# Kernel tuning notes

Measured on AMD Instinct MI355X. Metric: run time of the kernel, lower is better.

## Reference

```python
import jax, jax.numpy as jnp
import numpy as np

D_MODEL = 1024
NUM_HEADS = 16
MAX_SEQ_LEN = 2048
THETA = 10000.0
HEAD_DIM = D_MODEL // NUM_HEADS  # 64


def _trunc_normal(key, shape, std):
    # truncated normal in [-3, 3] sigma, matching nn.init.trunc_normal_
    return std * jax.random.truncated_normal(key, -3.0, 3.0, shape, dtype=jnp.float32)


def setup_inputs() -> dict:
    key = jax.random.key(0)
    kx, kq, kk, kv, ko = jax.random.split(key, 5)
    B, L = 2, 2048
    sigma = np.sqrt(2.0 / (D_MODEL + D_MODEL))
    x = jax.random.normal(kx, (B, L, D_MODEL), dtype=jnp.float32)
    token_positions = jnp.arange(L, dtype=jnp.int64 if jax.config.jax_enable_x64 else jnp.int32)[None, :]
    return {
        "x": x,
        "wq": _trunc_normal(kq, (D_MODEL, D_MODEL), sigma),
        "wk": _trunc_normal(kk, (D_MODEL, D_MODEL), sigma),
        "wv": _trunc_normal(kv, (D_MODEL, D_MODEL), sigma),
        "wo": _trunc_normal(ko, (D_MODEL, D_MODEL), sigma),
        "token_positions": token_positions,
    }


def _rope_tables():
    pos = jnp.arange(MAX_SEQ_LEN, dtype=jnp.float32)
    d_idx = jnp.arange(HEAD_DIM // 2, dtype=jnp.float32)
    inv_freq = THETA ** (-2.0 * d_idx / HEAD_DIM)
    angles = pos[:, None] * inv_freq[None, :]  # [max_seq_len, head_dim/2]
    return jnp.cos(angles), jnp.sin(angles)


def _apply_rope(x, cos, sin):
    # x: [b, n, l, h]; cos/sin: [1, l, h/2] (broadcast over b, n)
    xe = x[..., 0::2]
    xo = x[..., 1::2]
    oe = cos * xe - sin * xo
    oo = sin * xe + cos * xo
    # interleave back: stack last axis then flatten pairs
    out = jnp.stack([oe, oo], axis=-1)
    return out.reshape(x.shape)


def reference(x, wq, wk, wv, wo, token_positions):
    B, L, _ = x.shape
    cos_t, sin_t = _rope_tables()
    cos = cos_t[token_positions]  # [1, L, h/2]
    sin = sin_t[token_positions]

    def proj(w):
        y = jnp.einsum('bld,ed->ble', x, w)
        return y.reshape(B, L, NUM_HEADS, HEAD_DIM).transpose(0, 2, 1, 3)  # b n l h

    q, k, v = proj(wq), proj(wk), proj(wv)
    q = _apply_rope(q, cos, sin)
    k = _apply_rope(k, cos, sin)

    scale = 1.0 / np.sqrt(HEAD_DIM).astype(np.float32)
    logits = jnp.einsum('bnqh,bnkh->bnqk', q, k) * scale
    causal = jnp.tril(jnp.ones((L, L), dtype=bool))
    logits = jnp.where(causal[None, None], logits, -jnp.inf)
    scores = jax.nn.softmax(logits, axis=-1)
    out = jnp.einsum('bnqk,bnkh->bnqh', scores, v)
    out = out.transpose(0, 2, 1, 3).reshape(B, L, D_MODEL)
    return jnp.einsum('bld,ed->ble', out, wo)
```

## Files before the change

kernel.cpp:

```cpp
#include <hip/hip_runtime.h>
#include <stdint.h>
#include <stddef.h>

#define SEQ   2048
#define HD    64
#define DM    1024
#define NHEAD 16

typedef __bf16 bf16x8 __attribute__((ext_vector_type(8)));
typedef __bf16 bf16x4 __attribute__((ext_vector_type(4)));
typedef float  f32x4  __attribute__((ext_vector_type(4)));

#define MFMA16x16(a, b, c) __builtin_amdgcn_mfma_f32_16x16x32_bf16((a), (b), (c), 0, 0, 0)

__device__ __forceinline__ void gload16(const void* g, void* lds_uniform) {
    __builtin_amdgcn_global_load_lds(
        (const __attribute__((address_space(1))) uint32_t*)g,
        (__attribute__((address_space(3))) uint32_t*)lds_uniform, 16, 0, 0);
}

__global__ void prep_kernel(const float* __restrict__ x,
                            const float* __restrict__ wq, const float* __restrict__ wk,
                            const float* __restrict__ wv, const float* __restrict__ wo,
                            __bf16* __restrict__ xb, __bf16* __restrict__ wqkv,
                            __bf16* __restrict__ wob,
                            float* __restrict__ ct, float* __restrict__ st) {
    int bid = blockIdx.x;
    if (bid < 4096) {
        int i = (bid * 256 + threadIdx.x) * 4;
        const float4 v = *(const float4*)(x + i);
        __bf16 o[4] = {(__bf16)v.x, (__bf16)v.y, (__bf16)v.z, (__bf16)v.w};
        *(uint64_t*)(xb + i) = *(const uint64_t*)o;
    } else if (bid < 8192) {
        int g = (bid - 4096) >> 10;
        int i = (((bid - 4096) & 1023) * 256 + threadIdx.x) * 4;
        const float* src = (g == 0) ? wq : (g == 1) ? wk : (g == 2) ? wv : wo;
        __bf16* dst = (g == 3) ? wob : (wqkv + (size_t)g * 1048576);
        const float4 v = *(const float4*)(src + i);
        __bf16 o[4] = {(__bf16)v.x, (__bf16)v.y, (__bf16)v.z, (__bf16)v.w};
        *(uint64_t*)(dst + i) = *(const uint64_t*)o;
    } else {
        int i = (bid - 8192) * 256 + threadIdx.x;
        int p = i & 31;
        int pos = i >> 5;
        float freq = expf(-(float)p * (logf(10000.0f) / 32.0f));
        float ang = (float)pos * freq;
        ct[i] = cosf(ang);
        st[i] = sinf(ang);
    }
}

template <int MODE, int BN>
__global__ __launch_bounds__(256, 4)
void gemm_bt_kernel(const __bf16* __restrict__ A, const __bf16* __restrict__ W,
                    float* __restrict__ C, __bf16* __restrict__ Qb,
                    __bf16* __restrict__ Kb, __bf16* __restrict__ VTb,
                    const int* __restrict__ tpos, const float* __restrict__ ct,
                    const float* __restrict__ st, int N, int K) {
    constexpr int NJ = BN >> 5;
    __shared__ __align__(16) char smem[16384 + BN * 128];
    char* As = smem;
    char* Bs = smem + 16384;
    const int lane = threadIdx.x & 63;
    const int w    = threadIdx.x >> 6;

    const int nbn = N / BN;
    const int per = (nbn * 32) >> 3;
    const int id  = blockIdx.x;
    const int lin = (id & 7) * per + (id >> 3);
    const int bm  = lin / nbn;
    const int bn  = lin % nbn;

    const int rbase = (w >> 1) * 64;
    const int cbase = (w & 1) * (BN / 2);

    f32x4 acc[4][NJ] = {};

    const int kt_iters = K >> 6;
    for (int kt = 0; kt < kt_iters; ++kt) {
        #pragma unroll
        for (int c = 0; c < 4; ++c) {
            int id2 = (c * 4 + w) * 64 + lane;
            int row = id2 >> 3, cc = id2 & 7;
            int koff = kt * 64 + ((cc ^ (row & 7)) << 3);
            gload16(A + (size_t)(bm * 128 + row) * K + koff, As + (c * 4 + w) * 1024);
        }
        #pragma unroll
        for (int c = 0; c < NJ; ++c) {
            int id2 = (c * 4 + w) * 64 + lane;
            int row = id2 >> 3, cc = id2 & 7;
            int koff = kt * 64 + ((cc ^ (row & 7)) << 3);
            gload16(W + (size_t)(bn * BN + row) * K + koff, Bs + (c * 4 + w) * 1024);
        }
        __syncthreads();
        #pragma unroll
        for (int ks = 0; ks < 2; ++ks) {
            bf16x8 af[4], bfr[NJ];
            #pragma unroll
            for (int i = 0; i < 4; ++i) {
                int row = rbase + i * 16 + (lane & 15);
                int c = ks * 4 + (lane >> 4);
                af[i] = *(const bf16x8*)(As + row * 128 + ((c ^ (row & 7)) << 4));
            }
            #pragma unroll
            for (int j = 0; j < NJ; ++j) {
                int row = cbase + j * 16 + (lane & 15);
                int c = ks * 4 + (lane >> 4);
                bfr[j] = *(const bf16x8*)(Bs + row * 128 + ((c ^ (row & 7)) << 4));
            }
            #pragma unroll
            for (int i = 0; i < 4; ++i)
                #pragma unroll
                for (int j = 0; j < NJ; ++j)
                    acc[i][j] = MFMA16x16(af[i], bfr[j], acc[i][j]);
        }
        __syncthreads();
    }

    if (MODE == 1) {
        #pragma unroll
        for (int i = 0; i < 4; ++i)
            #pragma unroll
            for (int j = 0; j < NJ; ++j)
                #pragma unroll
                for (int r = 0; r < 4; ++r) {
                    int m = bm * 128 + rbase + i * 16 + (lane >> 4) * 4 + r;
                    int n = bn * BN + cbase + j * 16 + (lane & 15);
                    C[(size_t)m * N + n] = acc[i][j][r];
                }
    } else {
        const int which = bn >> 3;
        char* T = smem + w * 8192;
        #pragma unroll
        for (int i = 0; i < 4; ++i)
            #pragma unroll
            for (int j = 0; j < NJ; ++j)
                #pragma unroll
                for (int r = 0; r < 4; ++r) {
                    int mi = i * 16 + (lane >> 4) * 4 + r;
                    int ni = j * 16 + (lane & 15);
                    __bf16 v = (__bf16)acc[i][j][r];
                    if (which == 2)
                        *(__bf16*)(T + ni * 128 + ((mi * 2) ^ ((ni & 7) << 4))) = v;
                    else
                        *(__bf16*)(T + mi * 128 + ((ni * 2) ^ ((mi & 7) << 4))) = v;
                }
        #pragma unroll
        for (int it = 0; it < 8; ++it) {
            int id2 = it * 64 + lane;
            int row = id2 >> 3, cc = id2 & 7;
            bf16x8 v = *(const bf16x8*)(T + row * 128 + ((cc ^ (row & 7)) << 4));
            if (which == 2) {
                int n = bn * BN + cbase + row;
                int m = bm * 128 + rbase + cc * 8;
                int b = m >> 11, l = m & (SEQ - 1);
                int h = (n & (DM - 1)) >> 6, d = n & 63;
                *(bf16x8*)(VTb + ((size_t)((b * NHEAD + h) * HD + d) * SEQ) + l) = v;
            } else {
                int m = bm * 128 + rbase + row;
                int n = bn * BN + cbase + cc * 8;
                int b = m >> 11, l = m & (SEQ - 1);
                int h = (n & (DM - 1)) >> 6, d = n & 63;
                int pb = tpos[l] * 32 + (d >> 1);
                float sc = (which == 0) ? 0.18033688011112042f : 1.0f;
                bf16x8 ov;
                #pragma unroll
                for (int jj = 0; jj < 4; ++jj) {
                    float cs = ct[pb + jj], sn = st[pb + jj];
                    float e = (float)v[2 * jj], dd = (float)v[2 * jj + 1];
                    ov[2 * jj]     = (__bf16)(sc * (cs * e - sn * dd));
                    ov[2 * jj + 1] = (__bf16)(sc * (sn * e + cs * dd));
                }
                __bf16* dst = which ? Kb : Qb;
                *(bf16x8*)(dst + ((size_t)(b * NHEAD + h) * SEQ + l) * HD + d) = ov;
            }
        }
    }
}

__global__ __launch_bounds__(256, 4)
void attn_kernel(const __bf16* __restrict__ Q, const __bf16* __restrict__ K,
                 const __bf16* __restrict__ VT, __bf16* __restrict__ O) {
    __shared__ __align__(16) char smem[40960];
    const int lane = threadIdx.x & 63;
    const int w    = threadIdx.x >> 6;
    const int tid  = threadIdx.x;
    char* Ps = smem + 32768 + w * 2048;

    const int bid = blockIdx.x;
    const int xcd = bid & 7;
    const int idx = bid >> 3;
    const int s   = idx & 31;
    const int r   = idx >> 5;
    const int bh  = xcd * 4 + r;
    const int qb  = (r & 1) ? s : (31 - s);

    const __bf16* Qbh  = Q  + (size_t)bh * SEQ * HD;
    const __bf16* Kbh  = K  + (size_t)bh * SEQ * HD;
    const __bf16* VTbh = VT + (size_t)bh * HD * SEQ;
    const int b = bh >> 4, h = bh & 15;

    #pragma unroll
    for (int c = 0; c < 2; ++c) {
        int id = (c * 4 + w) * 64 + lane;
        int row = id >> 3, cc = id & 7;
        int sw = (cc ^ (row & 7)) << 3;
        gload16(Kbh + (size_t)row * HD + sw, smem + (c * 4 + w) * 1024);
        gload16(VTbh + (size_t)row * SEQ + sw, smem + 8192 + (c * 4 + w) * 1024);
    }

    const int qrow = qb * 64 + w * 16 + (lane & 15);
    bf16x8 qf[2];
    qf[0] = *(const bf16x8*)(Qbh + (size_t)qrow * HD + (lane >> 4) * 8);
    qf[1] = *(const bf16x8*)(Qbh + (size_t)qrow * HD + 32 + (lane >> 4) * 8);

    bf16x8 ones;
    #pragma unroll
    for (int i = 0; i < 8; ++i) ones[i] = (__bf16)1.0f;

    f32x4 o[4] = {};
    f32x4 ls = {};
    float mrow = -1e30f;

    int cur = 0;
    __syncthreads();

    for (int kb = 0; kb <= qb; ++kb) {
        bf16x8 kreg[2], vreg[2];
        if (kb < qb) {
            #pragma unroll
            for (int c = 0; c < 2; ++c) {
                int id = c * 256 + tid;
                int row = id >> 3, cc = id & 7;
                kreg[c] = *(const bf16x8*)(Kbh + (size_t)((kb + 1) * 64 + row) * HD + cc * 8);
                vreg[c] = *(const bf16x8*)(VTbh + (size_t)row * SEQ + (kb + 1) * 64 + cc * 8);
            }
        }

        char* Ks = smem + cur * 16384;
        char* Vs = Ks + 8192;

        f32x4 s4[4];
        __builtin_amdgcn_s_setprio(1);
        #pragma unroll
        for (int jt = 0; jt < 4; ++jt) {
            f32x4 z = {};
            #pragma unroll
            for (int ks = 0; ks < 2; ++ks) {
                int row = jt * 16 + (lane & 15);
                int c = ks * 4 + (lane >> 4);
                bf16x8 kf = *(const bf16x8*)(Ks + row * 128 + ((c ^ (row & 7)) << 4));
                z = MFMA16x16(kf, qf[ks], z);
            }
            s4[jt] = z;
        }
        __builtin_amdgcn_s_setprio(0);

        if (kb == qb) {
            int i = qb * 64 + w * 16 + (lane & 15);
            #pragma unroll
            for (int jt = 0; jt < 4; ++jt)
                #pragma unroll
                for (int rr = 0; rr < 4; ++rr) {
                    int j = kb * 64 + jt * 16 + (lane >> 4) * 4 + rr;
                    if (j > i) s4[jt][rr] = -1e30f;
                }
        }

        float t0 = fmaxf(fmaxf(fmaxf(s4[0][0], s4[0][1]), s4[0][2]), s4[0][3]);
        float t1 = fmaxf(fmaxf(fmaxf(s4[1][0], s4[1][1]), s4[1][2]), s4[1][3]);
        float t2 = fmaxf(fmaxf(fmaxf(s4[2][0], s4[2][1]), s4[2][2]), s4[2][3]);
        float t3 = fmaxf(fmaxf(fmaxf(s4[3][0], s4[3][1]), s4[3][2]), s4[3][3]);
        float pmax = fmaxf(fmaxf(fmaxf(t0, t1), t2), t3);

        if (!__all(pmax <= mrow + 8.0f)) {
            pmax = fmaxf(pmax, __shfl_xor(pmax, 16));
            pmax = fmaxf(pmax, __shfl_xor(pmax, 32));
            float mn = fmaxf(mrow, pmax);
            float alpha = exp2f(mrow - mn);
            mrow = mn;
            float ar[4];
            #pragma unroll
            for (int rr = 0; rr < 4; ++rr) ar[rr] = __shfl(alpha, (lane >> 4) * 4 + rr);
            #pragma unroll
            for (int rr = 0; rr < 4; ++rr) ls[rr] *= ar[rr];
            #pragma unroll
            for (int dt = 0; dt < 4; ++dt)
                #pragma unroll
                for (int rr = 0; rr < 4; ++rr)
                    o[dt][rr] *= ar[rr];
        }

        {
            int qr = lane & 15;
            int swrow = (qr & 7) << 4;
            #pragma unroll
            for (int jt = 0; jt < 4; ++jt) {
                bf16x4 pk;
                #pragma unroll
                for (int rr = 0; rr < 4; ++rr)
                    pk[rr] = (__bf16)exp2f(s4[jt][rr] - mrow);
                int jj = (jt * 16 + (lane >> 4) * 4) * 2;
                *(bf16x4*)(Ps + qr * 128 + (jj ^ swrow)) = pk;
            }
        }

        if (kb < qb) {
            char* Kn = smem + (cur ^ 1) * 16384;
            char* Vn = Kn + 8192;
            #pragma unroll
            for (int c = 0; c < 2; ++c) {
                int id = c * 256 + tid;
                int row = id >> 3, cc = id & 7;
                int sw = (cc ^ (row & 7)) << 4;
                *(bf16x8*)(Kn + row * 128 + sw) = kreg[c];
                *(bf16x8*)(Vn + row * 128 + sw) = vreg[c];
            }
        }

        __builtin_amdgcn_s_setprio(1);
        #pragma unroll
        for (int js = 0; js < 2; ++js) {
            int prow = lane & 15;
            int cb = js * 4 + (lane >> 4);
            bf16x8 pf = *(const bf16x8*)(Ps + prow * 128 + ((cb ^ (prow & 7)) << 4));
            ls = MFMA16x16(pf, ones, ls);
            #pragma unroll
            for (int dt = 0; dt < 4; ++dt) {
                int vrow = dt * 16 + (lane & 15);
                bf16x8 vf = *(const bf16x8*)(Vs + vrow * 128 + ((cb ^ (vrow & 7)) << 4));
                o[dt] = MFMA16x16(pf, vf, o[dt]);
            }
        }
        __builtin_amdgcn_s_setprio(0);

        __syncthreads();
        cur ^= 1;
    }

    float linv[4];
    #pragma unroll
    for (int rr = 0; rr < 4; ++rr) linv[rr] = 1.0f / ls[rr];

    char* Os = smem + 32768;
    #pragma unroll
    for (int dt = 0; dt < 4; ++dt)
        #pragma unroll
        for (int rr = 0; rr < 4; ++rr) {
            int orow = w * 16 + (lane >> 4) * 4 + rr;
            int oc = (dt * 16 + (lane & 15)) * 2;
            *(__bf16*)(Os + orow * 128 + (oc ^ ((orow & 7) << 4))) = (__bf16)(o[dt][rr] * linv[rr]);
        }
    __syncthreads();

    #pragma unroll
    for (int c = 0; c < 2; ++c) {
        int id = c * 256 + tid;
        int row = id >> 3, cc = id & 7;
        bf16x8 v = *(const bf16x8*)(Os + row * 128 + ((cc ^ (row & 7)) << 4));
        *(bf16x8*)(O + (size_t)(b * SEQ + qb * 64 + row) * DM + h * HD + cc * 8) = v;
    }
}

extern "C" void kernel_launch(void* const* d_in, const int* in_sizes, int n_in,
                              void* d_out, int out_size, void* d_ws, size_t ws_size,
                              hipStream_t stream) {
    const float* x  = (const float*)d_in[0];
    const float* wq = (const float*)d_in[1];
    const float* wk = (const float*)d_in[2];
    const float* wv = (const float*)d_in[3];
    const float* wo = (const float*)d_in[4];
    const int* tpos = (const int*)d_in[5];
    float* out = (float*)d_out;
    char* ws = (char*)d_ws;

    __bf16* xb   = (__bf16*)(ws);
    __bf16* wqkv = (__bf16*)(ws + (size_t)(8  << 20));
    __bf16* wob  = (__bf16*)(ws + (size_t)(14 << 20));
    __bf16* Qb   = (__bf16*)(ws + (size_t)(16 << 20));
    __bf16* Kb   = (__bf16*)(ws + (size_t)(24 << 20));
    __bf16* VTb  = (__bf16*)(ws + (size_t)(32 << 20));
    __bf16* Ob   = (__bf16*)(ws + (size_t)(40 << 20));
    float* ct    = (float*)(ws + (size_t)(48 << 20));
    float* st    = (float*)(ws + (size_t)(48 << 20) + 262144);

    prep_kernel<<<8448, 256, 0, stream>>>(x, wq, wk, wv, wo, xb, wqkv, wob, ct, st);
    gemm_bt_kernel<0, 128><<<768, 256, 0, stream>>>(xb, wqkv, nullptr, Qb, Kb, VTb,
                                                    tpos, ct, st, 3072, 1024);
    attn_kernel<<<1024, 256, 0, stream>>>(Qb, Kb, VTb, Ob);
    gemm_bt_kernel<1, 64><<<512, 256, 0, stream>>>(Ob, wob, out, nullptr, nullptr, nullptr,
                                                   nullptr, nullptr, nullptr, 1024, 1024);
}
```

Baseline: 103.4 us.

## Process 128 query rows per attention block to reuse K/V tiles

The attention kernel now gives each wave two 16-row query fragments, so a block covers 128 query rows instead of 64. Each K/V tile loaded into LDS feeds twice as many MFMAs, and the grid is halved to 512 blocks with a new head/query-tile mapping for causal load balancing. Waves whose rows lie entirely before a KV tile skip compute for that tile. The cost is more registers and LDS, with launch bounds lowered to 2 blocks per SM, so occupancy drops and causal imbalance per block grows.

```diff
diff --git a/kernel.cpp b/kernel.cpp
--- a/kernel.cpp
+++ b/kernel.cpp
@@ -178,27 +178,32 @@
     }
 }
 
-__global__ __launch_bounds__(256, 4)
+__global__ __launch_bounds__(256, 2)
 void attn_kernel(const __bf16* __restrict__ Q, const __bf16* __restrict__ K,
                  const __bf16* __restrict__ VT, __bf16* __restrict__ O) {
-    __shared__ __align__(16) char smem[40960];
+    __shared__ __align__(16) char smem[49152];
     const int lane = threadIdx.x & 63;
     const int w    = threadIdx.x >> 6;
     const int tid  = threadIdx.x;
-    char* Ps = smem + 32768 + w * 2048;
+    const int hi   = lane >> 4;
+    const int lo   = lane & 15;
+    char* Ps = smem + 32768 + w * 4096;
 
     const int bid = blockIdx.x;
     const int xcd = bid & 7;
     const int idx = bid >> 3;
-    const int s   = idx & 31;
-    const int r   = idx >> 5;
-    const int bh  = xcd * 4 + r;
-    const int qb  = (r & 1) ? s : (31 - s);
+    int hl, qt;
+    if (idx < 32) { hl = idx & 1;       qt = 15 - (idx >> 1); }
+    else          { hl = 2 + (idx & 1); qt = (idx - 32) >> 1; }
+    const int bh = xcd * 4 + hl;
 
     const __bf16* Qbh  = Q  + (size_t)bh * SEQ * HD;
     const __bf16* Kbh  = K  + (size_t)bh * SEQ * HD;
     const __bf16* VTbh = VT + (size_t)bh * HD * SEQ;
     const int b = bh >> 4, h = bh & 15;
+
+    const int nkv  = 2 * qt + 2;
+    const int iBase = qt * 128 + w * 32;
 
     #pragma unroll
     for (int c = 0; c < 2; ++c) {
@@ -209,25 +214,28 @@
         gload16(VTbh + (size_t)row * SEQ + sw, smem + 8192 + (c * 4 + w) * 1024);
     }
 
-    const int qrow = qb * 64 + w * 16 + (lane & 15);
-    bf16x8 qf[2];
-    qf[0] = *(const bf16x8*)(Qbh + (size_t)qrow * HD + (lane >> 4) * 8);
-    qf[1] = *(const bf16x8*)(Qbh + (size_t)qrow * HD + 32 + (lane >> 4) * 8);
+    bf16x8 qf[2][2];
+    #pragma unroll
+    for (int f = 0; f < 2; ++f) {
+        int qrow = iBase + f * 16 + lo;
+        qf[f][0] = *(const bf16x8*)(Qbh + (size_t)qrow * HD + hi * 8);
+        qf[f][1] = *(const bf16x8*)(Qbh + (size_t)qrow * HD + 32 + hi * 8);
+    }
 
     bf16x8 ones;
     #pragma unroll
     for (int i = 0; i < 8; ++i) ones[i] = (__bf16)1.0f;
 
-    f32x4 o[4] = {};
-    f32x4 ls = {};
-    float mrow = -1e30f;
+    f32x4 o0[4] = {}, o1[4] = {};
+    f32x4 ls0 = {}, ls1 = {};
+    float mrow0 = -1e30f, mrow1 = -1e30f;
 
     int cur = 0;
     __syncthreads();
 
-    for (int kb = 0; kb <= qb; ++kb) {
+    for (int kb = 0; kb < nkv; ++kb) {
         bf16x8 kreg[2], vreg[2];
-        if (kb < qb) {
+        if (kb + 1 < nkv) {
             #pragma unroll
             for (int c = 0; c < 2; ++c) {
                 int id = c * 256 + tid;
@@ -240,72 +248,109 @@
         char* Ks = smem + cur * 16384;
         char* Vs = Ks + 8192;
 
-        f32x4 s4[4];
-        __builtin_amdgcn_s_setprio(1);
-        #pragma unroll
-        for (int jt = 0; jt < 4; ++jt) {
-            f32x4 z = {};
-            #pragma unroll
-            for (int ks = 0; ks < 2; ++ks) {
-                int row = jt * 16 + (lane & 15);
-                int c = ks * 4 + (lane >> 4);
-                bf16x8 kf = *(const bf16x8*)(Ks + row * 128 + ((c ^ (row & 7)) << 4));
-                z = MFMA16x16(kf, qf[ks], z);
-            }
-            s4[jt] = z;
-        }
-        __builtin_amdgcn_s_setprio(0);
-
-        if (kb == qb) {
-            int i = qb * 64 + w * 16 + (lane & 15);
-            #pragma unroll
-            for (int jt = 0; jt < 4; ++jt)
-                #pragma unroll
-                for (int rr = 0; rr < 4; ++rr) {
-                    int j = kb * 64 + jt * 16 + (lane >> 4) * 4 + rr;
-                    if (j > i) s4[jt][rr] = -1e30f;
-                }
-        }
-
-        float t0 = fmaxf(fmaxf(fmaxf(s4[0][0], s4[0][1]), s4[0][2]), s4[0][3]);
-        float t1 = fmaxf(fmaxf(fmaxf(s4[1][0], s4[1][1]), s4[1][2]), s4[1][3]);
-        float t2 = fmaxf(fmaxf(fmaxf(s4[2][0], s4[2][1]), s4[2][2]), s4[2][3]);
-        float t3 = fmaxf(fmaxf(fmaxf(s4[3][0], s4[3][1]), s4[3][2]), s4[3][3]);
-        float pmax = fmaxf(fmaxf(fmaxf(t0, t1), t2), t3);
-
-        if (!__all(pmax <= mrow + 8.0f)) {
-            pmax = fmaxf(pmax, __shfl_xor(pmax, 16));
-            pmax = fmaxf(pmax, __shfl_xor(pmax, 32));
-            float mn = fmaxf(mrow, pmax);
-            float alpha = exp2f(mrow - mn);
-            mrow = mn;
-            float ar[4];
-            #pragma unroll
-            for (int rr = 0; rr < 4; ++rr) ar[rr] = __shfl(alpha, (lane >> 4) * 4 + rr);
-            #pragma unroll
-            for (int rr = 0; rr < 4; ++rr) ls[rr] *= ar[rr];
-            #pragma unroll
-            for (int dt = 0; dt < 4; ++dt)
-                #pragma unroll
-                for (int rr = 0; rr < 4; ++rr)
-                    o[dt][rr] *= ar[rr];
-        }
-
-        {
-            int qr = lane & 15;
-            int swrow = (qr & 7) << 4;
+        const bool active = (kb * 64) <= (iBase + 31);
+
+        if (active) {
+            f32x4 s0[4], s1[4];
+            __builtin_amdgcn_s_setprio(1);
             #pragma unroll
             for (int jt = 0; jt < 4; ++jt) {
-                bf16x4 pk;
-                #pragma unroll
-                for (int rr = 0; rr < 4; ++rr)
-                    pk[rr] = (__bf16)exp2f(s4[jt][rr] - mrow);
-                int jj = (jt * 16 + (lane >> 4) * 4) * 2;
-                *(bf16x4*)(Ps + qr * 128 + (jj ^ swrow)) = pk;
-            }
-        }
-
-        if (kb < qb) {
+                f32x4 z0 = {}, z1 = {};
+                #pragma unroll
+                for (int ks = 0; ks < 2; ++ks) {
+                    int row = jt * 16 + lo;
+                    int c = ks * 4 + hi;
+                    bf16x8 kf = *(const bf16x8*)(Ks + row * 128 + ((c ^ (row & 7)) << 4));
+                    z0 = MFMA16x16(kf, qf[0][ks], z0);
+                    z1 = MFMA16x16(kf, qf[1][ks], z1);
+                }
+                s0[jt] = z0;
+                s1[jt] = z1;
+            }
+            __builtin_amdgcn_s_setprio(0);
+
+            if (kb * 64 + 63 > iBase) {
+                int i0 = iBase + lo, i1 = iBase + 16 + lo;
+                #pragma unroll
+                for (int jt = 0; jt < 4; ++jt)
+                    #pragma unroll
+                    for (int rr = 0; rr < 4; ++rr) {
+                        int j = kb * 64 + jt * 16 + hi * 4 + rr;
+                        if (j > i0) s0[jt][rr] = -1e30f;
+                        if (j > i1) s1[jt][rr] = -1e30f;
+                    }
+            }
+
+            float a0 = fmaxf(fmaxf(fmaxf(s0[0][0], s0[0][1]), s0[0][2]), s0[0][3]);
+            float a1 = fmaxf(fmaxf(fmaxf(s0[1][0], s0[1][1]), s0[1][2]), s0[1][3]);
+            float a2 = fmaxf(fmaxf(fmaxf(s0[2][0], s0[2][1]), s0[2][2]), s0[2][3]);
+            float a3 = fmaxf(fmaxf(fmaxf(s0[3][0], s0[3][1]), s0[3][2]), s0[3][3]);
+            float pmax0 = fmaxf(fmaxf(a0, a1), fmaxf(a2, a3));
+            float b0 = fmaxf(fmaxf(fmaxf(s1[0][0], s1[0][1]), s1[0][2]), s1[0][3]);
+            float b1 = fmaxf(fmaxf(fmaxf(s1[1][0], s1[1][1]), s1[1][2]), s1[1][3]);
+            float b2 = fmaxf(fmaxf(fmaxf(s1[2][0], s1[2][1]), s1[2][2]), s1[2][3]);
+            float b3 = fmaxf(fmaxf(fmaxf(s1[3][0], s1[3][1]), s1[3][2]), s1[3][3]);
+            float pmax1 = fmaxf(fmaxf(b0, b1), fmaxf(b2, b3));
+
+            if (!__all(pmax0 <= mrow0 + 8.0f && pmax1 <= mrow1 + 8.0f)) {
+                {
+                    float pm = fmaxf(pmax0, __shfl_xor(pmax0, 16));
+                    pm = fmaxf(pm, __shfl_xor(pm, 32));
+                    float mn = fmaxf(mrow0, pm);
+                    float alpha = exp2f(mrow0 - mn);
+                    mrow0 = mn;
+                    float ar[4];
+                    #pragma unroll
+                    for (int rr = 0; rr < 4; ++rr) ar[rr] = __shfl(alpha, hi * 4 + rr);
+                    #pragma unroll
+                    for (int rr = 0; rr < 4; ++rr) ls0[rr] *= ar[rr];
+                    #pragma unroll
+                    for (int dt = 0; dt < 4; ++dt)
+                        #pragma unroll
+                        for (int rr = 0; rr < 4; ++rr) o0[dt][rr] *= ar[rr];
+                }
+                {
+                    float pm = fmaxf(pmax1, __shfl_xor(pmax1, 16));
+                    pm = fmaxf(pm, __shfl_xor(pm, 32));
+                    float mn = fmaxf(mrow1, pm);
+                    float alpha = exp2f(mrow1 - mn);
+                    mrow1 = mn;
+                    float ar[4];
+                    #pragma unroll
+                    for (int rr = 0; rr < 4; ++rr) ar[rr] = __shfl(alpha, hi * 4 + rr);
+                    #pragma unroll
+                    for (int rr = 0; rr < 4; ++rr) ls1[rr] *= ar[rr];
+                    #pragma unroll
+                    for (int dt = 0; dt < 4; ++dt)
+                        #pragma unroll
+                        for (int rr = 0; rr < 4; ++rr) o1[dt][rr] *= ar[rr];
+                }
+            }
+
+            {
+                int swr = (lo & 7) << 4;
+                #pragma unroll
+                for (int jt = 0; jt < 4; ++jt) {
+                    bf16x4 pk;
+                    #pragma unroll
+                    for (int rr = 0; rr < 4; ++rr)
+                        pk[rr] = (__bf16)exp2f(s0[jt][rr] - mrow0);
+                    int jj = (jt * 16 + hi * 4) * 2;
+                    *(bf16x4*)(Ps + lo * 128 + (jj ^ swr)) = pk;
+                }
+                #pragma unroll
+                for (int jt = 0; jt < 4; ++jt) {
+                    bf16x4 pk;
+                    #pragma unroll
+                    for (int rr = 0; rr < 4; ++rr)
+                        pk[rr] = (__bf16)exp2f(s1[jt][rr] - mrow1);
+                    int jj = (jt * 16 + hi * 4) * 2;
+                    *(bf16x4*)(Ps + (16 + lo) * 128 + (jj ^ swr)) = pk;
+                }
+            }
+        }
+
+        if (kb + 1 < nkv) {
             char* Kn = smem + (cur ^ 1) * 16384;
             char* Vn = Kn + 8192;
             #pragma unroll
@@ -318,47 +363,54 @@
             }
         }
 
-        __builtin_amdgcn_s_setprio(1);
-        #pragma unroll
-        for (int js = 0; js < 2; ++js) {
-            int prow = lane & 15;
-            int cb = js * 4 + (lane >> 4);
-            bf16x8 pf = *(const bf16x8*)(Ps + prow * 128 + ((cb ^ (prow & 7)) << 4));
-            ls = MFMA16x16(pf, ones, ls);
-            #pragma unroll
-            for (int dt = 0; dt < 4; ++dt) {
-                int vrow = dt * 16 + (lane & 15);
-                bf16x8 vf = *(const bf16x8*)(Vs + vrow * 128 + ((cb ^ (vrow & 7)) << 4));
-                o[dt] = MFMA16x16(pf, vf, o[dt]);
-            }
-        }
-        __builtin_amdgcn_s_setprio(0);
+        if (active) {
+            __builtin_amdgcn_s_setprio(1);
+            #pragma unroll
+            for (int js = 0; js < 2; ++js) {
+                int cb = js * 4 + hi;
+                int sw = ((cb ^ (lo & 7)) << 4);
+                bf16x8 pf0 = *(const bf16x8*)(Ps + lo * 128 + sw);
+                bf16x8 pf1 = *(const bf16x8*)(Ps + (16 + lo) * 128 + sw);
+                ls0 = MFMA16x16(pf0, ones, ls0);
+                ls1 = MFMA16x16(pf1, ones, ls1);
+                #pragma unroll
+                for (int dt = 0; dt < 4; ++dt) {
+                    int vrow = dt * 16 + lo;
+                    bf16x8 vf = *(const bf16x8*)(Vs + vrow * 128 + ((cb ^ (vrow & 7)) << 4));
+                    o0[dt] = MFMA16x16(pf0, vf, o0[dt]);
+                    o1[dt] = MFMA16x16(pf1, vf, o1[dt]);
+                }
+            }
+            __builtin_amdgcn_s_setprio(0);
+        }
 
         __syncthreads();
         cur ^= 1;
     }
 
-    float linv[4];
-    #pragma unroll
-    for (int rr = 0; rr < 4; ++rr) linv[rr] = 1.0f / ls[rr];
+    float linv0[4], linv1[4];
+    #pragma unroll
+    for (int rr = 0; rr < 4; ++rr) { linv0[rr] = 1.0f / ls0[rr]; linv1[rr] = 1.0f / ls1[rr]; }
 
     char* Os = smem + 32768;
     #pragma unroll
     for (int dt = 0; dt < 4; ++dt)
         #pragma unroll
         for (int rr = 0; rr < 4; ++rr) {
-            int orow = w * 16 + (lane >> 4) * 4 + rr;
-            int oc = (dt * 16 + (lane & 15)) * 2;
-            *(__bf16*)(Os + orow * 128 + (oc ^ ((orow & 7) << 4))) = (__bf16)(o[dt][rr] * linv[rr]);
+            int orow0 = w * 32 + hi * 4 + rr;
+            int orow1 = orow0 + 16;
+            int oc = (dt * 16 + lo) * 2;
+            *(__bf16*)(Os + orow0 * 128 + (oc ^ ((orow0 & 7) << 4))) = (__bf16)(o0[dt][rr] * linv0[rr]);
+            *(__bf16*)(Os + orow1 * 128 + (oc ^ ((orow1 & 7) << 4))) = (__bf16)(o1[dt][rr] * linv1[rr]);
         }
     __syncthreads();
 
     #pragma unroll
-    for (int c = 0; c < 2; ++c) {
+    for (int c = 0; c < 4; ++c) {
         int id = c * 256 + tid;
         int row = id >> 3, cc = id & 7;
         bf16x8 v = *(const bf16x8*)(Os + row * 128 + ((cc ^ (row & 7)) << 4));
-        *(bf16x8*)(O + (size_t)(b * SEQ + qb * 64 + row) * DM + h * HD + cc * 8) = v;
+        *(bf16x8*)(O + (size_t)(b * SEQ + qt * 128 + row) * DM + h * HD + cc * 8) = v;
     }
 }
 
@@ -387,7 +439,7 @@
     prep_kernel<<<8448, 256, 0, stream>>>(x, wq, wk, wv, wo, xb, wqkv, wob, ct, st);
     gemm_bt_kernel<0, 128><<<768, 256, 0, stream>>>(xb, wqkv, nullptr, Qb, Kb, VTb,
                                                     tpos, ct, st, 3072, 1024);
-    attn_kernel<<<1024, 256, 0, stream>>>(Qb, Kb, VTb, Ob);
+    attn_kernel<<<512, 256, 0, stream>>>(Qb, Kb, VTb, Ob);
     gemm_bt_kernel<1, 64><<<512, 256, 0, stream>>>(Ob, wob, out, nullptr, nullptr, nullptr,
                                                    nullptr, nullptr, nullptr, 1024, 1024);
 }
```

After: 111.7 us. 1.08x slower.

## Load K/V fragments directly from global into registers, drop LDS staging

Applied to the files above, without the earlier changes.

Removes the double-buffered LDS staging of K and V tiles and the per-iteration block barrier. Each wave now loads its MFMA K and V^T fragments straight from global memory (served from L2/L1), and LDS shrinks to 8 KB for P and the output tile. This cuts LDS traffic and synchronisation, and the smaller footprint may allow higher occupancy. In exchange, each of the four waves re-reads the same K/V data from global memory and there is no explicit prefetch to hide load latency.

```diff
diff --git a/kernel.cpp b/kernel.cpp
--- a/kernel.cpp
+++ b/kernel.cpp
@@ -181,11 +181,13 @@
 __global__ __launch_bounds__(256, 4)
 void attn_kernel(const __bf16* __restrict__ Q, const __bf16* __restrict__ K,
                  const __bf16* __restrict__ VT, __bf16* __restrict__ O) {
-    __shared__ __align__(16) char smem[40960];
+    __shared__ __align__(16) char smem[8192];
     const int lane = threadIdx.x & 63;
     const int w    = threadIdx.x >> 6;
     const int tid  = threadIdx.x;
-    char* Ps = smem + 32768 + w * 2048;
+    const int hi   = lane >> 4;
+    const int lo   = lane & 15;
+    char* Ps = smem + w * 2048;
 
     const int bid = blockIdx.x;
     const int xcd = bid & 7;
@@ -200,19 +202,10 @@
     const __bf16* VTbh = VT + (size_t)bh * HD * SEQ;
     const int b = bh >> 4, h = bh & 15;
 
-    #pragma unroll
-    for (int c = 0; c < 2; ++c) {
-        int id = (c * 4 + w) * 64 + lane;
-        int row = id >> 3, cc = id & 7;
-        int sw = (cc ^ (row & 7)) << 3;
-        gload16(Kbh + (size_t)row * HD + sw, smem + (c * 4 + w) * 1024);
-        gload16(VTbh + (size_t)row * SEQ + sw, smem + 8192 + (c * 4 + w) * 1024);
-    }
-
-    const int qrow = qb * 64 + w * 16 + (lane & 15);
+    const int qrow = qb * 64 + w * 16 + lo;
     bf16x8 qf[2];
-    qf[0] = *(const bf16x8*)(Qbh + (size_t)qrow * HD + (lane >> 4) * 8);
-    qf[1] = *(const bf16x8*)(Qbh + (size_t)qrow * HD + 32 + (lane >> 4) * 8);
+    qf[0] = *(const bf16x8*)(Qbh + (size_t)qrow * HD + hi * 8);
+    qf[1] = *(const bf16x8*)(Qbh + (size_t)qrow * HD + 32 + hi * 8);
 
     bf16x8 ones;
     #pragma unroll
@@ -222,23 +215,22 @@
     f32x4 ls = {};
     float mrow = -1e30f;
 
-    int cur = 0;
-    __syncthreads();
-
     for (int kb = 0; kb <= qb; ++kb) {
-        bf16x8 kreg[2], vreg[2];
-        if (kb < qb) {
-            #pragma unroll
-            for (int c = 0; c < 2; ++c) {
-                int id = c * 256 + tid;
-                int row = id >> 3, cc = id & 7;
-                kreg[c] = *(const bf16x8*)(Kbh + (size_t)((kb + 1) * 64 + row) * HD + cc * 8);
-                vreg[c] = *(const bf16x8*)(VTbh + (size_t)row * SEQ + (kb + 1) * 64 + cc * 8);
-            }
-        }
-
-        char* Ks = smem + cur * 16384;
-        char* Vs = Ks + 8192;
+        bf16x8 kfr[4][2];
+        #pragma unroll
+        for (int jt = 0; jt < 4; ++jt)
+            #pragma unroll
+            for (int ks = 0; ks < 2; ++ks)
+                kfr[jt][ks] = *(const bf16x8*)(
+                    Kbh + (size_t)(kb * 64 + jt * 16 + lo) * HD + (ks * 4 + hi) * 8);
+
+        bf16x8 vfr[2][4];
+        #pragma unroll
+        for (int js = 0; js < 2; ++js)
+            #pragma unroll
+            for (int dt = 0; dt < 4; ++dt)
+                vfr[js][dt] = *(const bf16x8*)(
+                    VTbh + (size_t)(dt * 16 + lo) * SEQ + kb * 64 + (js * 4 + hi) * 8);
 
         f32x4 s4[4];
         __builtin_amdgcn_s_setprio(1);
@@ -246,23 +238,19 @@
         for (int jt = 0; jt < 4; ++jt) {
             f32x4 z = {};
             #pragma unroll
-            for (int ks = 0; ks < 2; ++ks) {
-                int row = jt * 16 + (lane & 15);
-                int c = ks * 4 + (lane >> 4);
-                bf16x8 kf = *(const bf16x8*)(Ks + row * 128 + ((c ^ (row & 7)) << 4));
-                z = MFMA16x16(kf, qf[ks], z);
-            }
+            for (int ks = 0; ks < 2; ++ks)
+                z = MFMA16x16(kfr[jt][ks], qf[ks], z);
             s4[jt] = z;
         }
         __builtin_amdgcn_s_setprio(0);
 
         if (kb == qb) {
-            int i = qb * 64 + w * 16 + (lane & 15);
+            int i = qb * 64 + w * 16 + lo;
             #pragma unroll
             for (int jt = 0; jt < 4; ++jt)
                 #pragma unroll
                 for (int rr = 0; rr < 4; ++rr) {
-                    int j = kb * 64 + jt * 16 + (lane >> 4) * 4 + rr;
+                    int j = kb * 64 + jt * 16 + hi * 4 + rr;
                     if (j > i) s4[jt][rr] = -1e30f;
                 }
         }
@@ -281,7 +269,7 @@
             mrow = mn;
             float ar[4];
             #pragma unroll
-            for (int rr = 0; rr < 4; ++rr) ar[rr] = __shfl(alpha, (lane >> 4) * 4 + rr);
+            for (int rr = 0; rr < 4; ++rr) ar[rr] = __shfl(alpha, hi * 4 + rr);
             #pragma unroll
             for (int rr = 0; rr < 4; ++rr) ls[rr] *= ar[rr];
             #pragma unroll
@@ -292,63 +280,42 @@
         }
 
         {
-            int qr = lane & 15;
-            int swrow = (qr & 7) << 4;
+            int swr = (lo & 7) << 4;
             #pragma unroll
             for (int jt = 0; jt < 4; ++jt) {
                 bf16x4 pk;
                 #pragma unroll
                 for (int rr = 0; rr < 4; ++rr)
                     pk[rr] = (__bf16)exp2f(s4[jt][rr] - mrow);
-                int jj = (jt * 16 + (lane >> 4) * 4) * 2;
-                *(bf16x4*)(Ps + qr * 128 + (jj ^ swrow)) = pk;
+                int jj = (jt * 16 + hi * 4) * 2;
+                *(bf16x4*)(Ps + lo * 128 + (jj ^ swr)) = pk;
             }
         }
 
-        if (kb < qb) {
-            char* Kn = smem + (cur ^ 1) * 16384;
-            char* Vn = Kn + 8192;
-            #pragma unroll
-            for (int c = 0; c < 2; ++c) {
-                int id = c * 256 + tid;
-                int row = id >> 3, cc = id & 7;
-                int sw = (cc ^ (row & 7)) << 4;
-                *(bf16x8*)(Kn + row * 128 + sw) = kreg[c];
-                *(bf16x8*)(Vn + row * 128 + sw) = vreg[c];
-            }
-        }
-
         __builtin_amdgcn_s_setprio(1);
         #pragma unroll
         for (int js = 0; js < 2; ++js) {
-            int prow = lane & 15;
-            int cb = js * 4 + (lane >> 4);
-            bf16x8 pf = *(const bf16x8*)(Ps + prow * 128 + ((cb ^ (prow & 7)) << 4));
+            int cb = js * 4 + hi;
+            bf16x8 pf = *(const bf16x8*)(Ps + lo * 128 + ((cb ^ (lo & 7)) << 4));
             ls = MFMA16x16(pf, ones, ls);
             #pragma unroll
-            for (int dt = 0; dt < 4; ++dt) {
-                int vrow = dt * 16 + (lane & 15);
-                bf16x8 vf = *(const bf16x8*)(Vs + vrow * 128 + ((cb ^ (vrow & 7)) << 4));
-                o[dt] = MFMA16x16(pf, vf, o[dt]);
-            }
+            for (int dt = 0; dt < 4; ++dt)
+                o[dt] = MFMA16x16(pf, vfr[js][dt], o[dt]);
         }
         __builtin_amdgcn_s_setprio(0);
-
-        __syncthreads();
-        cur ^= 1;
     }
 
     float linv[4];
     #pragma unroll
     for (int rr = 0; rr < 4; ++rr) linv[rr] = 1.0f / ls[rr];
 
-    char* Os = smem + 32768;
+    char* Os = smem;
     #pragma unroll
     for (int dt = 0; dt < 4; ++dt)
         #pragma unroll
         for (int rr = 0; rr < 4; ++rr) {
-            int orow = w * 16 + (lane >> 4) * 4 + rr;
-            int oc = (dt * 16 + (lane & 15)) * 2;
+            int orow = w * 16 + hi * 4 + rr;
+            int oc = (dt * 16 + lo) * 2;
             *(__bf16*)(Os + orow * 128 + (oc ^ ((orow & 7) << 4))) = (__bf16)(o[dt][rr] * linv[rr]);
         }
     __syncthreads();
```

After: 180.4 us. 74.5% more time.
